# Optimization experiments

Hardware: AMD Instinct MI355X
Metric: run time of the kernel (lower is better)

Reference implementation:

```python
import jax, jax.numpy as jnp
import numpy as np

B, D, N = 32768, 128, 8
TEMP = 0.25          # episodic_memory_temperature
DECAY = 0.99         # episodic_strength_decay
AGE_INC = 0.02       # episodic_age_increment


def _l2norm(x, eps=1e-6):
    n = jnp.sqrt(jnp.sum(x * x, axis=-1, keepdims=True))
    return x / jnp.maximum(n, eps)


def setup_inputs() -> dict:
    key = jax.random.key(0)
    ks = jax.random.split(key, 16)
    s = 0.05
    inp = {
        'signal': jax.random.normal(ks[0], (B, D), jnp.float32),
        'previous': jax.random.normal(ks[1], (B, D), jnp.float32),
        'hidden': jax.random.normal(ks[2], (B, D), jnp.float32),
        'episodic_keys': jax.random.normal(ks[3], (B, N, D), jnp.float32),
        'episodic_values': jax.random.normal(ks[4], (B, N, D), jnp.float32),
        'episodic_strength': jax.random.uniform(ks[5], (B, N), jnp.float32),
        'episodic_age': jax.random.uniform(ks[6], (B, N), jnp.float32),
        # Linear weights stored as [in, out] (torch stores [out, in]); small random
        # instead of the zero init so gradients flow for kernel testing.
        'w_read_query': jax.random.normal(ks[7], (2 * D, D), jnp.float32) * s,
        'w_read_mix': jax.random.normal(ks[8], (2 * D, 1), jnp.float32) * s,
        'b_read_mix': jnp.full((1,), -0.2, jnp.float32),
        'w_key': jax.random.normal(ks[9], (2 * D, D), jnp.float32) * s,
        'b_key': jnp.zeros((D,), jnp.float32),
        'w_value': jax.random.normal(ks[10], (2 * D, D), jnp.float32) * s,
        'b_value': jnp.zeros((D,), jnp.float32),
        'w_write': jax.random.normal(ks[11], (2 * D, 1), jnp.float32) * s,
        'b_write': jnp.full((1,), -0.6, jnp.float32),
        'w_persist': jax.random.normal(ks[12], (2 * D, 1), jnp.float32) * s,
        'b_persist': jnp.zeros((1,), jnp.float32),
        'w_merge': jax.random.normal(ks[13], (2 * D, 1), jnp.float32) * s,
        'b_merge': jnp.zeros((1,), jnp.float32),
    }
    return inp


def reference(signal, previous, hidden, episodic_keys, episodic_values,
              episodic_strength, episodic_age,
              w_read_query, w_read_mix, b_read_mix, w_key, b_key, w_value,
              b_value, w_write, b_write, w_persist, b_persist, w_merge, b_merge):
    dtype = signal.dtype
    n_slots = episodic_keys.shape[1]

    # ---------------- read ----------------
    sp = jnp.concatenate([signal, previous], axis=-1)             # [B, 2D]
    query = _l2norm(sp @ w_read_query)                            # [B, D]
    norm_keys = _l2norm(episodic_keys)                            # [B, N, D]
    content_scores = jnp.einsum('bd,bnd->bn', query, norm_keys)   # [B, N]
    content_w = jax.nn.softmax(content_scores / TEMP, axis=-1)
    content_read = jnp.einsum('bn,bnd->bd', content_w, episodic_values)
    persistent_scores = 2.4 * episodic_strength + 0.6 * (1.0 - episodic_age)
    persistent_w = jax.nn.softmax(persistent_scores / TEMP, axis=-1)
    persistent_read = jnp.einsum('bn,bnd->bd', persistent_w, episodic_values)
    read_mix = jax.nn.sigmoid(sp @ w_read_mix + b_read_mix)       # [B, 1]
    memory_read = read_mix * content_read + (1.0 - read_mix) * persistent_read

    # ---------------- write ----------------
    joined = jnp.concatenate([signal, hidden], axis=-1)           # [B, 2D]
    candidate_key = jnp.tanh(joined @ w_key + b_key)              # [B, D]
    candidate_value = jnp.tanh(joined @ w_value + b_value)        # [B, D]
    write_strength = jax.nn.sigmoid(joined @ w_write + b_write)   # [B, 1]
    persistence = jax.nn.sigmoid(joined @ w_persist + b_persist)  # [B, 1]
    similarity = jnp.einsum('bd,bnd->bn', _l2norm(candidate_key), norm_keys)

    top_k = min(3, n_slots)
    top_sim, top_idx = jax.lax.top_k(similarity, top_k)           # [B, 3]
    max_sim = top_sim[:, 0]
    merge_index = top_idx[:, 0]
    second_sim = top_sim[:, 1]
    novelty = jnp.clip(1.0 - max_sim, 0.0, 1.0)[:, None]          # [B, 1]

    replace_scores = (1.2 * episodic_age + 1.0 * (1.0 - episodic_strength)
                      + 0.5 * (1.0 - similarity))
    replace_index = jnp.argmax(replace_scores, axis=-1)
    merge_pref = jax.nn.sigmoid(joined @ w_merge + b_merge + 2.6 * max_sim[:, None])

    full_m = (max_sim > 0.78) & (merge_pref[:, 0] >= 0.55)
    multi_m = full_m & (second_sim > 0.68)
    partial_m = (~multi_m) & (max_sim > 0.64) & (second_sim > 0.52)

    rows = jnp.arange(signal.shape[0])[:, None]
    target_w = jax.nn.one_hot(replace_index, n_slots, dtype=dtype)
    partial_w = jax.nn.softmax(top_sim[:, :2] / TEMP, axis=-1)
    partial_target = jnp.zeros_like(target_w).at[rows, top_idx[:, :2]].add(partial_w)
    multi_w = jax.nn.softmax(top_sim / TEMP, axis=-1)
    multi_target = jnp.zeros_like(target_w).at[rows, top_idx].add(multi_w)
    full_target = jax.nn.one_hot(merge_index, n_slots, dtype=dtype)

    target_w = jnp.where(full_m[:, None], full_target, target_w)
    target_w = jnp.where(partial_m[:, None], partial_target, target_w)
    target_w = jnp.where(multi_m[:, None], multi_target, target_w)

    scale = jnp.where(multi_m[:, None], 0.16 + 0.52 * write_strength,
                      jnp.where(partial_m[:, None], 0.18 + 0.62 * write_strength,
                                0.20 + 0.80 * write_strength))
    overwrite = target_w * scale * (0.55 + 0.45 * novelty)        # [B, N]
    ow3 = overwrite[..., None]                                    # [B, N, 1]

    merge_like = full_m | partial_m | multi_m
    key_mix = jnp.where(merge_like[:, None], 0.28 + 0.24 * persistence,
                        0.78 + 0.16 * persistence)[:, :, None]    # [B, 1, 1]
    value_mix = jnp.where(merge_like[:, None], 0.42 + 0.28 * persistence,
                          0.82 + 0.12 * persistence)[:, :, None]

    updated_keys = episodic_keys + ow3 * key_mix * (candidate_key[:, None, :] - episodic_keys)
    updated_values = episodic_values + ow3 * value_mix * (candidate_value[:, None, :] - episodic_values)

    boost = overwrite * (0.45 + 0.35 * persistence + 0.45 * novelty + 0.25 * write_strength)
    updated_strength = jnp.clip(episodic_strength * DECAY + boost, 0.0, 1.0)
    updated_age = jnp.clip((episodic_age + AGE_INC) * (1.0 - overwrite), 0.0, 1.0)

    return memory_read, updated_keys, updated_values, updated_strength, updated_age
```

## Files before the change

kernel.cpp:

```cpp
#include <hip/hip_runtime.h>
#include <cstddef>

#define BD 128
#define NS 8
#define ROWS 4
#define BLOCK 256

typedef float __attribute__((ext_vector_type(4))) f32x4;
typedef float __attribute__((ext_vector_type(2))) f32x2;

__device__ __forceinline__ float sigm(float x) { return 1.0f / (1.0f + __expf(-x)); }

__device__ __forceinline__ void nt_store2(float2 v, float2* p) {
    f32x2 t; t.x = v.x; t.y = v.y;
    __builtin_nontemporal_store(t, (f32x2*)p);
}

__global__ __launch_bounds__(BLOCK, 3)
void sbcore_kernel(
    const float* __restrict__ g_signal, const float* __restrict__ g_prev,
    const float* __restrict__ g_hidden, const float* __restrict__ g_keys,
    const float* __restrict__ g_vals, const float* __restrict__ g_str,
    const float* __restrict__ g_age,
    const float* __restrict__ w_rq, const float* __restrict__ w_mix,
    const float* __restrict__ b_mix, const float* __restrict__ w_key,
    const float* __restrict__ b_key, const float* __restrict__ w_val,
    const float* __restrict__ b_val, const float* __restrict__ w_wr,
    const float* __restrict__ b_wr, const float* __restrict__ w_pe,
    const float* __restrict__ b_pe, const float* __restrict__ w_mg,
    const float* __restrict__ b_mg,
    float* __restrict__ o_read, float* __restrict__ o_keys,
    float* __restrict__ o_vals, float* __restrict__ o_str,
    float* __restrict__ o_age)
{
    __shared__ __align__(16) float sig_s[ROWS][BD];
    __shared__ __align__(16) float prv_s[ROWS][BD];
    __shared__ __align__(16) float hid_s[ROWS][BD];
    __shared__ __align__(16) f32x4 part_s[4][3][ROWS][32];
    __shared__ float str_s[ROWS*NS], age_s[ROWS*NS];
    __shared__ __align__(16) float head_s[ROWS][4];

    const int tid = threadIdx.x;
    const int row0 = blockIdx.x * ROWS;

    if (tid < ROWS*32) {
        int r = tid >> 5, d4 = tid & 31;
        size_t gb = (size_t)(row0 + r) * 32 + d4;
        *(float4*)&sig_s[r][d4*4] = ((const float4*)g_signal)[gb];
        *(float4*)&prv_s[r][d4*4] = ((const float4*)g_prev)[gb];
        *(float4*)&hid_s[r][d4*4] = ((const float4*)g_hidden)[gb];
    }
    if (tid < ROWS*NS) {
        str_s[tid] = g_str[(size_t)row0*NS + tid];
        age_s[tid] = g_age[(size_t)row0*NS + tid];
    }
    __syncthreads();

    {
        const int dotid = tid >> 4;
        const int hr = dotid >> 2;
        const int hh = dotid & 3;
        const int hj = tid & 15;
        const float* ws = (hh==0) ? w_mix : (hh==1) ? w_wr : (hh==2) ? w_pe : w_mg;
        const float* xb = (hj < 8) ? &sig_s[hr][0]
                        : (((hh==0) ? &prv_s[hr][0] : &hid_s[hr][0]) - BD);
        float p = 0.f;
#pragma unroll
        for (int q = 0; q < 4; ++q) {
            const int k = hj*16 + q*4;
            const float4 w4 = *(const float4*)&ws[k];
            const float4 x4 = *(const float4*)&xb[k];
            p = fmaf(x4.w, w4.w, fmaf(x4.z, w4.z, fmaf(x4.y, w4.y, fmaf(x4.x, w4.x, p))));
        }
        p += __shfl_xor(p, 1); p += __shfl_xor(p, 2);
        p += __shfl_xor(p, 4); p += __shfl_xor(p, 8);
        if (hj == 0) head_s[hr][hh] = p;
    }

    const int wave = tid >> 6;
    const int lane = tid & 63;
    const int hi   = lane >> 5;
    const int dg   = lane & 31;

    {
        const int kbase = hi ? (BD + wave*32) : (wave*32);
        const f32x4* wq4 = (const f32x4*)w_rq;
        const f32x4* wk4 = (const f32x4*)w_key;
        const f32x4* wv4 = (const f32x4*)w_val;
        const int wi0 = kbase*32 + dg;
        const float* x1b = hi ? &prv_s[0][0] : &sig_s[0][0];
        const float* x2b = hi ? &hid_s[0][0] : &sig_s[0][0];
        const int xo = wave*32;

        f32x4 aq[ROWS], ak[ROWS], av[ROWS];
#pragma unroll
        for (int r = 0; r < ROWS; ++r) { aq[r] = 0.f; ak[r] = 0.f; av[r] = 0.f; }

#pragma unroll 2
        for (int j = 0; j < 8; ++j) {
            const int kj = j*4;
            f32x4 w0 = wq4[wi0 + (kj+0)*32], w1 = wq4[wi0 + (kj+1)*32],
                  w2 = wq4[wi0 + (kj+2)*32], w3 = wq4[wi0 + (kj+3)*32];
#pragma unroll
            for (int r = 0; r < ROWS; ++r) {
                const f32x4 x1 = *(const f32x4*)&x1b[r*BD + xo + kj];
                aq[r] += x1.x*w0; aq[r] += x1.y*w1; aq[r] += x1.z*w2; aq[r] += x1.w*w3;
            }
            f32x4 k0 = wk4[wi0 + (kj+0)*32], k1 = wk4[wi0 + (kj+1)*32],
                  k2 = wk4[wi0 + (kj+2)*32], k3 = wk4[wi0 + (kj+3)*32];
            f32x4 v0 = wv4[wi0 + (kj+0)*32], v1 = wv4[wi0 + (kj+1)*32],
                  v2 = wv4[wi0 + (kj+2)*32], v3 = wv4[wi0 + (kj+3)*32];
#pragma unroll
            for (int r = 0; r < ROWS; ++r) {
                const f32x4 x2 = *(const f32x4*)&x2b[r*BD + xo + kj];
                ak[r] += x2.x*k0; ak[r] += x2.y*k1; ak[r] += x2.z*k2; ak[r] += x2.w*k3;
                av[r] += x2.x*v0; av[r] += x2.y*v1; av[r] += x2.z*v2; av[r] += x2.w*v3;
            }
        }

#pragma unroll
        for (int r = 0; r < ROWS; ++r) {
            f32x4 t;
            t.x = __shfl_xor(aq[r].x, 32); t.y = __shfl_xor(aq[r].y, 32);
            t.z = __shfl_xor(aq[r].z, 32); t.w = __shfl_xor(aq[r].w, 32);
            aq[r] += t;
            t.x = __shfl_xor(ak[r].x, 32); t.y = __shfl_xor(ak[r].y, 32);
            t.z = __shfl_xor(ak[r].z, 32); t.w = __shfl_xor(ak[r].w, 32);
            ak[r] += t;
            t.x = __shfl_xor(av[r].x, 32); t.y = __shfl_xor(av[r].y, 32);
            t.z = __shfl_xor(av[r].z, 32); t.w = __shfl_xor(av[r].w, 32);
            av[r] += t;
        }
        if (!hi) {
#pragma unroll
            for (int r = 0; r < ROWS; ++r) {
                part_s[wave][0][r][dg] = aq[r];
                part_s[wave][1][r][dg] = ak[r];
                part_s[wave][2][r][dg] = av[r];
            }
        }
    }
    __syncthreads();

    const int r = wave;
    float ckinv_reg;
    {
        const int dgf = lane >> 1;
        const int co  = (lane & 1) * 2;
        float2 sq = make_float2(0.f, 0.f), sk = make_float2(0.f, 0.f),
               sv = make_float2(0.f, 0.f);
#pragma unroll
        for (int pw = 0; pw < 4; ++pw) {
            const float* pq = (const float*)&part_s[pw][0][r][dgf];
            const float* pk = (const float*)&part_s[pw][1][r][dgf];
            const float* pv = (const float*)&part_s[pw][2][r][dgf];
            const float2 tq = *(const float2*)&pq[co];
            const float2 tk = *(const float2*)&pk[co];
            const float2 tv = *(const float2*)&pv[co];
            sq.x += tq.x; sq.y += tq.y;
            sk.x += tk.x; sk.y += tk.y;
            sv.x += tv.x; sv.y += tv.y;
        }
        const float2 bk2 = *(const float2*)&b_key[2*lane];
        const float2 bv2 = *(const float2*)&b_val[2*lane];
        const float ckx = tanhf(sk.x + bk2.x), cky = tanhf(sk.y + bk2.y);
        const float cvx = tanhf(sv.x + bv2.x), cvy = tanhf(sv.y + bv2.y);
        float q2 = sq.x*sq.x + sq.y*sq.y;
        float c2 = ckx*ckx + cky*cky;
#pragma unroll
        for (int off = 32; off > 0; off >>= 1) {
            q2 += __shfl_xor(q2, off);
            c2 += __shfl_xor(c2, off);
        }
        const float qinv = 1.0f / fmaxf(sqrtf(q2), 1e-6f);
        ckinv_reg = 1.0f / fmaxf(sqrtf(c2), 1e-6f);
        *(float2*)&sig_s[r][2*lane] = make_float2(sq.x*qinv, sq.y*qinv);
        *(float2*)&prv_s[r][2*lane] = make_float2(ckx, cky);
        *(float2*)&hid_s[r][2*lane] = make_float2(cvx, cvy);
    }
    __syncthreads();

    const float bmix = b_mix[0], bwr = b_wr[0], bpe = b_pe[0], bmg = b_mg[0];
    const int sj = lane & 7;
    {
        const size_t row = (size_t)row0 + r;
        const size_t kvb = row * (size_t)(NS*BD);

        const float4* kp4  = (const float4*)(g_keys + kvb);
        const float4* qrow = (const float4*)&sig_s[r][0];
        const float4* crow = (const float4*)&prv_s[r][0];
        float pk = 0.f, pq = 0.f, pc = 0.f;
#pragma unroll
        for (int q = 0; q < 4; ++q) {
            const float4 k4 = kp4[4*lane + q];
            const float4 q4 = qrow[sj*4 + q];
            const float4 c4 = crow[sj*4 + q];
            pk = fmaf(k4.w,k4.w, fmaf(k4.z,k4.z, fmaf(k4.y,k4.y, fmaf(k4.x,k4.x, pk))));
            pq = fmaf(q4.w,k4.w, fmaf(q4.z,k4.z, fmaf(q4.y,k4.y, fmaf(q4.x,k4.x, pq))));
            pc = fmaf(c4.w,k4.w, fmaf(c4.z,k4.z, fmaf(c4.y,k4.y, fmaf(c4.x,k4.x, pc))));
        }
        const float2* vp = (const float2*)(g_vals + kvb);
        float2 vf[NS];
#pragma unroll
        for (int n = 0; n < NS; ++n) vf[n] = vp[n*64 + lane];
        const float2 cki = *(const float2*)&prv_s[r][2*lane];
        const float2 cvi = *(const float2*)&hid_s[r][2*lane];

        pk += __shfl_xor(pk, 1); pk += __shfl_xor(pk, 2); pk += __shfl_xor(pk, 4);
        pq += __shfl_xor(pq, 1); pq += __shfl_xor(pq, 2); pq += __shfl_xor(pq, 4);
        pc += __shfl_xor(pc, 1); pc += __shfl_xor(pc, 2); pc += __shfl_xor(pc, 4);
        const float ki   = 1.0f / fmaxf(sqrtf(pk), 1e-6f);
        const float csn  = pq * ki;
        const float simn = pc * ki * ckinv_reg;
        float cs[NS], sim[NS];
#pragma unroll
        for (int m = 0; m < NS; ++m) {
            cs[m]  = __shfl(csn,  m*8);
            sim[m] = __shfl(simn, m*8);
        }

        const float4 hd = *(const float4*)&head_s[r][0];
        const float mix   = sigm(hd.x + bmix);
        const float wsv   = sigm(hd.y + bwr);
        const float pev   = sigm(hd.z + bpe);
        const float mglin = hd.w + bmg;

        float mC = cs[0];
#pragma unroll
        for (int n = 1; n < NS; ++n) mC = fmaxf(mC, cs[n]);
        float eC[NS], sC = 0.f;
#pragma unroll
        for (int n = 0; n < NS; ++n) { eC[n] = __expf((cs[n]-mC)*4.0f); sC += eC[n]; }
        const float4 st0 = *(const float4*)&str_s[r*NS];
        const float4 st1 = *(const float4*)&str_s[r*NS+4];
        const float4 ag0 = *(const float4*)&age_s[r*NS];
        const float4 ag1 = *(const float4*)&age_s[r*NS+4];
        const float stv[NS] = {st0.x,st0.y,st0.z,st0.w,st1.x,st1.y,st1.z,st1.w};
        const float agv[NS] = {ag0.x,ag0.y,ag0.z,ag0.w,ag1.x,ag1.y,ag1.z,ag1.w};
        float psc[NS]; float mP = -1e30f;
#pragma unroll
        for (int n = 0; n < NS; ++n) {
            psc[n] = fmaf(2.4f, stv[n], 0.6f*(1.0f - agv[n]));
            mP = fmaxf(mP, psc[n]);
        }
        float eP[NS], sP = 0.f;
#pragma unroll
        for (int n = 0; n < NS; ++n) { eP[n] = __expf((psc[n]-mP)*4.0f); sP += eP[n]; }
        const float icS = 1.0f/sC, ipS = 1.0f/sP;

        float2 cr = make_float2(0.f, 0.f), prd = make_float2(0.f, 0.f);
#pragma unroll
        for (int n = 0; n < NS; ++n) {
            float wc = eC[n]*icS, wp = eP[n]*ipS;
            cr.x  = fmaf(wc, vf[n].x, cr.x);  cr.y  = fmaf(wc, vf[n].y, cr.y);
            prd.x = fmaf(wp, vf[n].x, prd.x); prd.y = fmaf(wp, vf[n].y, prd.y);
        }
        float2 mr;
        mr.x = mix*cr.x + (1.0f-mix)*prd.x;
        mr.y = mix*cr.y + (1.0f-mix)*prd.y;
        nt_store2(mr, &((float2*)(o_read + row*BD))[lane]);

        float tv0 = -1e30f; int ti0 = 0;
#pragma unroll
        for (int n = 0; n < NS; ++n) if (sim[n] > tv0) { tv0 = sim[n]; ti0 = n; }
        float tv1 = -1e30f; int ti1 = 0;
#pragma unroll
        for (int n = 0; n < NS; ++n) {
            float v = (n == ti0) ? -1e30f : sim[n];
            if (v > tv1) { tv1 = v; ti1 = n; }
        }
        float tv2 = -1e30f; int ti2 = 0;
#pragma unroll
        for (int n = 0; n < NS; ++n) {
            float v = (n == ti0 || n == ti1) ? -1e30f : sim[n];
            if (v > tv2) { tv2 = v; ti2 = n; }
        }

        float rm = -1e30f; int ri = 0;
#pragma unroll
        for (int n = 0; n < NS; ++n) {
            float rsv = fmaf(1.2f, agv[n], (1.0f - stv[n])) + 0.5f*(1.0f - sim[n]);
            if (rsv > rm) { rm = rsv; ri = n; }
        }

        const float mpref = sigm(mglin + 2.6f*tv0);
        const bool full  = (tv0 > 0.78f) && (mpref >= 0.55f);
        const bool multi = full && (tv1 > 0.68f);
        const bool part  = (!multi) && (tv0 > 0.64f) && (tv1 > 0.52f);
        const float nov  = fminf(fmaxf(1.0f - tv0, 0.0f), 1.0f);

        float a0, a1, a2, aR;
        if (multi) {
            float e1 = __expf((tv1 - tv0)*4.0f), e2 = __expf((tv2 - tv0)*4.0f);
            float inv = 1.0f/(1.0f + e1 + e2);
            a0 = inv; a1 = e1*inv; a2 = e2*inv; aR = 0.f;
        } else if (part) {
            float e1 = __expf((tv1 - tv0)*4.0f);
            float inv = 1.0f/(1.0f + e1);
            a0 = inv; a1 = e1*inv; a2 = 0.f; aR = 0.f;
        } else if (full) {
            a0 = 1.f; a1 = 0.f; a2 = 0.f; aR = 0.f;
        } else {
            a0 = 0.f; a1 = 0.f; a2 = 0.f; aR = 1.f;
        }

        const float scl = multi ? fmaf(0.52f, wsv, 0.16f)
                        : part  ? fmaf(0.62f, wsv, 0.18f)
                                : fmaf(0.80f, wsv, 0.20f);
        const bool  mlike = full || part || multi;
        const float km  = mlike ? fmaf(0.24f, pev, 0.28f) : fmaf(0.16f, pev, 0.78f);
        const float vm  = mlike ? fmaf(0.28f, pev, 0.42f) : fmaf(0.12f, pev, 0.82f);
        const float owc = scl * fmaf(0.45f, nov, 0.55f);
        const float bco = 0.45f + 0.35f*pev + 0.45f*nov + 0.25f*wsv;

        const float2* kp2 = (const float2*)(g_keys + kvb);
        float2* okp = (float2*)(o_keys + kvb);
        float2* ovp = (float2*)(o_vals + kvb);
#pragma unroll
        for (int n = 0; n < NS; ++n) {
            const float2 kf2 = kp2[n*64 + lane];
            float tn = ((n==ti0) ? a0 : (n==ti1) ? a1 : (n==ti2) ? a2 : 0.f)
                     + ((n==ri) ? aR : 0.f);
            float ow = tn*owc;
            float a = ow*km, b2 = ow*vm;
            float2 uk, uv;
            uk.x = fmaf(a,  cki.x - kf2.x, kf2.x);
            uk.y = fmaf(a,  cki.y - kf2.y, kf2.y);
            uv.x = fmaf(b2, cvi.x - vf[n].x, vf[n].x);
            uv.y = fmaf(b2, cvi.y - vf[n].y, vf[n].y);
            nt_store2(uk, &okp[n*64 + lane]);
            nt_store2(uv, &ovp[n*64 + lane]);
        }
        if (lane < NS) {
            float tn = ((lane==ti0) ? a0 : (lane==ti1) ? a1 : (lane==ti2) ? a2 : 0.f)
                     + ((lane==ri) ? aR : 0.f);
            float ow = tn*owc;
            float us = fminf(fmaxf(fmaf(str_s[r*NS+lane], 0.99f, ow*bco), 0.f), 1.f);
            float ua = fminf(fmaxf((age_s[r*NS+lane] + 0.02f)*(1.0f - ow), 0.f), 1.f);
            o_str[row*NS + lane] = us;
            o_age[row*NS + lane] = ua;
        }
    }
}

extern "C" void kernel_launch(void* const* d_in, const int* in_sizes, int n_in,
                              void* d_out, int out_size, void* d_ws, size_t ws_size,
                              hipStream_t stream) {
    const float* g_signal = (const float*)d_in[0];
    const float* g_prev   = (const float*)d_in[1];
    const float* g_hidden = (const float*)d_in[2];
    const float* g_keys   = (const float*)d_in[3];
    const float* g_vals   = (const float*)d_in[4];
    const float* g_str    = (const float*)d_in[5];
    const float* g_age    = (const float*)d_in[6];
    const float* w_rq     = (const float*)d_in[7];
    const float* w_mix    = (const float*)d_in[8];
    const float* b_mix    = (const float*)d_in[9];
    const float* w_key    = (const float*)d_in[10];
    const float* b_key    = (const float*)d_in[11];
    const float* w_val    = (const float*)d_in[12];
    const float* b_val    = (const float*)d_in[13];
    const float* w_wr     = (const float*)d_in[14];
    const float* b_wr     = (const float*)d_in[15];
    const float* w_pe     = (const float*)d_in[16];
    const float* b_pe     = (const float*)d_in[17];
    const float* w_mg     = (const float*)d_in[18];
    const float* b_mg     = (const float*)d_in[19];

    const size_t B = (size_t)in_sizes[0] / BD;
    float* out   = (float*)d_out;
    float* o_read = out;
    float* o_keys = o_read + B*BD;
    float* o_vals = o_keys + B*NS*BD;
    float* o_str  = o_vals + B*NS*BD;
    float* o_age  = o_str  + B*NS;

    const int blocks = (int)(B / ROWS);
    sbcore_kernel<<<dim3(blocks), dim3(BLOCK), 0, stream>>>(
        g_signal, g_prev, g_hidden, g_keys, g_vals, g_str, g_age,
        w_rq, w_mix, b_mix, w_key, b_key, w_val, b_val,
        w_wr, b_wr, w_pe, b_pe, w_mg, b_mg,
        o_read, o_keys, o_vals, o_str, o_age);
}
```

Measured before the change: 613.3 us.

## Split fused kernel into matvec and slot-update kernels via workspace

Splits the single fused kernel into two: one computes the query/key/value projections, head logits and inverse norms into a workspace, and the other streams the episodic keys and values to do slot scoring, read and update. The fused kernel is kept as a fallback when no workspace is provided. The aim is to let each phase use its own resource profile (occupancy, memory streaming) instead of mixing compute-heavy matvec with bandwidth-bound slot traffic. It adds a workspace round trip of about 389 floats per row plus an extra launch.

```diff
diff --git a/kernel.cpp b/kernel.cpp
--- a/kernel.cpp
+++ b/kernel.cpp
@@ -17,7 +17,340 @@
 }
 
 __global__ __launch_bounds__(BLOCK, 3)
-void sbcore_kernel(
+void sbcore_matvec(
+    const float* __restrict__ g_signal, const float* __restrict__ g_prev,
+    const float* __restrict__ g_hidden,
+    const float* __restrict__ w_rq, const float* __restrict__ w_mix,
+    const float* __restrict__ w_key, const float* __restrict__ b_key,
+    const float* __restrict__ w_val, const float* __restrict__ b_val,
+    const float* __restrict__ w_wr, const float* __restrict__ w_pe,
+    const float* __restrict__ w_mg,
+    float* __restrict__ ws_qcv, float* __restrict__ ws_heads,
+    float* __restrict__ ws_ckinv)
+{
+    __shared__ __align__(16) float sig_s[ROWS][BD];
+    __shared__ __align__(16) float prv_s[ROWS][BD];
+    __shared__ __align__(16) float hid_s[ROWS][BD];
+    __shared__ __align__(16) f32x4 part_s[4][3][ROWS][32];
+
+    const int tid = threadIdx.x;
+    const int row0 = blockIdx.x * ROWS;
+    const int wave = tid >> 6;
+    const int lane = tid & 63;
+
+    if (tid < ROWS*32) {
+        int r = tid >> 5, d4 = tid & 31;
+        size_t gb = (size_t)(row0 + r) * 32 + d4;
+        *(float4*)&sig_s[r][d4*4] = ((const float4*)g_signal)[gb];
+        *(float4*)&prv_s[r][d4*4] = ((const float4*)g_prev)[gb];
+        *(float4*)&hid_s[r][d4*4] = ((const float4*)g_hidden)[gb];
+    }
+    __syncthreads();
+
+    {
+        const int dotid = tid >> 4;
+        const int hr = dotid >> 2;
+        const int hh = dotid & 3;
+        const int hj = tid & 15;
+        const float* ws = (hh==0) ? w_mix : (hh==1) ? w_wr : (hh==2) ? w_pe : w_mg;
+        const float* xb = (hj < 8) ? &sig_s[hr][0]
+                        : (((hh==0) ? &prv_s[hr][0] : &hid_s[hr][0]) - BD);
+        float p = 0.f;
+#pragma unroll
+        for (int q = 0; q < 4; ++q) {
+            const int k = hj*16 + q*4;
+            const float4 w4 = *(const float4*)&ws[k];
+            const float4 x4 = *(const float4*)&xb[k];
+            p = fmaf(x4.w, w4.w, fmaf(x4.z, w4.z, fmaf(x4.y, w4.y, fmaf(x4.x, w4.x, p))));
+        }
+        p += __shfl_xor(p, 1); p += __shfl_xor(p, 2);
+        p += __shfl_xor(p, 4); p += __shfl_xor(p, 8);
+        if (hj == 0) ws_heads[(size_t)(row0 + hr)*4 + hh] = p;
+    }
+
+    const int hi = lane >> 5;
+    const int dg = lane & 31;
+
+    {
+        const int kbase = hi ? (BD + wave*32) : (wave*32);
+        const f32x4* wq4 = (const f32x4*)w_rq;
+        const f32x4* wk4 = (const f32x4*)w_key;
+        const f32x4* wv4 = (const f32x4*)w_val;
+        const int wi0 = kbase*32 + dg;
+        const float* x1b = hi ? &prv_s[0][0] : &sig_s[0][0];
+        const float* x2b = hi ? &hid_s[0][0] : &sig_s[0][0];
+        const int xo = wave*32;
+
+        f32x4 aq[ROWS], ak[ROWS], av[ROWS];
+#pragma unroll
+        for (int r = 0; r < ROWS; ++r) { aq[r] = 0.f; ak[r] = 0.f; av[r] = 0.f; }
+
+#pragma unroll 2
+        for (int j = 0; j < 8; ++j) {
+            const int kj = j*4;
+            f32x4 w0 = wq4[wi0 + (kj+0)*32], w1 = wq4[wi0 + (kj+1)*32],
+                  w2 = wq4[wi0 + (kj+2)*32], w3 = wq4[wi0 + (kj+3)*32];
+#pragma unroll
+            for (int r = 0; r < ROWS; ++r) {
+                const f32x4 x1 = *(const f32x4*)&x1b[r*BD + xo + kj];
+                aq[r] += x1.x*w0; aq[r] += x1.y*w1; aq[r] += x1.z*w2; aq[r] += x1.w*w3;
+            }
+            f32x4 k0 = wk4[wi0 + (kj+0)*32], k1 = wk4[wi0 + (kj+1)*32],
+                  k2 = wk4[wi0 + (kj+2)*32], k3 = wk4[wi0 + (kj+3)*32];
+            f32x4 v0 = wv4[wi0 + (kj+0)*32], v1 = wv4[wi0 + (kj+1)*32],
+                  v2 = wv4[wi0 + (kj+2)*32], v3 = wv4[wi0 + (kj+3)*32];
+#pragma unroll
+            for (int r = 0; r < ROWS; ++r) {
+                const f32x4 x2 = *(const f32x4*)&x2b[r*BD + xo + kj];
+                ak[r] += x2.x*k0; ak[r] += x2.y*k1; ak[r] += x2.z*k2; ak[r] += x2.w*k3;
+                av[r] += x2.x*v0; av[r] += x2.y*v1; av[r] += x2.z*v2; av[r] += x2.w*v3;
+            }
+        }
+
+#pragma unroll
+        for (int r = 0; r < ROWS; ++r) {
+            f32x4 t;
+            t.x = __shfl_xor(aq[r].x, 32); t.y = __shfl_xor(aq[r].y, 32);
+            t.z = __shfl_xor(aq[r].z, 32); t.w = __shfl_xor(aq[r].w, 32);
+            aq[r] += t;
+            t.x = __shfl_xor(ak[r].x, 32); t.y = __shfl_xor(ak[r].y, 32);
+            t.z = __shfl_xor(ak[r].z, 32); t.w = __shfl_xor(ak[r].w, 32);
+            ak[r] += t;
+            t.x = __shfl_xor(av[r].x, 32); t.y = __shfl_xor(av[r].y, 32);
+            t.z = __shfl_xor(av[r].z, 32); t.w = __shfl_xor(av[r].w, 32);
+            av[r] += t;
+        }
+        if (!hi) {
+#pragma unroll
+            for (int r = 0; r < ROWS; ++r) {
+                part_s[wave][0][r][dg] = aq[r];
+                part_s[wave][1][r][dg] = ak[r];
+                part_s[wave][2][r][dg] = av[r];
+            }
+        }
+    }
+    __syncthreads();
+
+    const int r = wave;
+    {
+        const int dgf = lane >> 1;
+        const int co  = (lane & 1) * 2;
+        float2 sq = make_float2(0.f, 0.f), sk = make_float2(0.f, 0.f),
+               sv = make_float2(0.f, 0.f);
+#pragma unroll
+        for (int pw = 0; pw < 4; ++pw) {
+            const float* pq = (const float*)&part_s[pw][0][r][dgf];
+            const float* pk = (const float*)&part_s[pw][1][r][dgf];
+            const float* pv = (const float*)&part_s[pw][2][r][dgf];
+            const float2 tq = *(const float2*)&pq[co];
+            const float2 tk = *(const float2*)&pk[co];
+            const float2 tv = *(const float2*)&pv[co];
+            sq.x += tq.x; sq.y += tq.y;
+            sk.x += tk.x; sk.y += tk.y;
+            sv.x += tv.x; sv.y += tv.y;
+        }
+        const float2 bk2 = *(const float2*)&b_key[2*lane];
+        const float2 bv2 = *(const float2*)&b_val[2*lane];
+        const float ckx = tanhf(sk.x + bk2.x), cky = tanhf(sk.y + bk2.y);
+        const float cvx = tanhf(sv.x + bv2.x), cvy = tanhf(sv.y + bv2.y);
+        float q2 = sq.x*sq.x + sq.y*sq.y;
+        float c2 = ckx*ckx + cky*cky;
+#pragma unroll
+        for (int off = 32; off > 0; off >>= 1) {
+            q2 += __shfl_xor(q2, off);
+            c2 += __shfl_xor(c2, off);
+        }
+        const float qinv = 1.0f / fmaxf(sqrtf(q2), 1e-6f);
+        const size_t rowb = ((size_t)row0 + r) * 384;
+        *(float2*)&ws_qcv[rowb + 2*lane]       = make_float2(sq.x*qinv, sq.y*qinv);
+        *(float2*)&ws_qcv[rowb + 128 + 2*lane] = make_float2(ckx, cky);
+        *(float2*)&ws_qcv[rowb + 256 + 2*lane] = make_float2(cvx, cvy);
+        if (lane == 0) ws_ckinv[(size_t)row0 + r] = 1.0f / fmaxf(sqrtf(c2), 1e-6f);
+    }
+}
+
+__global__ __launch_bounds__(BLOCK, 2)
+void sbcore_slots(
+    const float* __restrict__ ws_qcv, const float* __restrict__ ws_heads,
+    const float* __restrict__ ws_ckinv,
+    const float* __restrict__ g_keys, const float* __restrict__ g_vals,
+    const float* __restrict__ g_str, const float* __restrict__ g_age,
+    const float* __restrict__ b_mix, const float* __restrict__ b_wr,
+    const float* __restrict__ b_pe, const float* __restrict__ b_mg,
+    float* __restrict__ o_read, float* __restrict__ o_keys,
+    float* __restrict__ o_vals, float* __restrict__ o_str,
+    float* __restrict__ o_age)
+{
+    const int tid  = threadIdx.x;
+    const int wave = tid >> 6;
+    const int lane = tid & 63;
+    const int sj   = lane & 7;
+    const size_t row = (size_t)blockIdx.x * ROWS + wave;
+    const size_t kvb = row * (size_t)(NS*BD);
+
+    const float* wsrow = ws_qcv + row*384;
+    const float4* qrow = (const float4*)wsrow;
+    const float4* crow = (const float4*)(wsrow + 128);
+    const float4* kp4  = (const float4*)(g_keys + kvb);
+    const float2* vp2  = (const float2*)(g_vals + kvb);
+
+    float pk = 0.f, pq = 0.f, pc = 0.f;
+#pragma unroll
+    for (int q = 0; q < 4; ++q) {
+        const float4 k4 = kp4[4*lane + q];
+        const float4 q4 = qrow[sj*4 + q];
+        const float4 c4 = crow[sj*4 + q];
+        pk = fmaf(k4.w,k4.w, fmaf(k4.z,k4.z, fmaf(k4.y,k4.y, fmaf(k4.x,k4.x, pk))));
+        pq = fmaf(q4.w,k4.w, fmaf(q4.z,k4.z, fmaf(q4.y,k4.y, fmaf(q4.x,k4.x, pq))));
+        pc = fmaf(c4.w,k4.w, fmaf(c4.z,k4.z, fmaf(c4.y,k4.y, fmaf(c4.x,k4.x, pc))));
+    }
+    float2 vf[NS];
+#pragma unroll
+    for (int n = 0; n < NS; ++n) vf[n] = vp2[n*64 + lane];
+    const float2 cki = ((const float2*)(wsrow + 128))[lane];
+    const float2 cvi = ((const float2*)(wsrow + 256))[lane];
+
+    pk += __shfl_xor(pk, 1); pk += __shfl_xor(pk, 2); pk += __shfl_xor(pk, 4);
+    pq += __shfl_xor(pq, 1); pq += __shfl_xor(pq, 2); pq += __shfl_xor(pq, 4);
+    pc += __shfl_xor(pc, 1); pc += __shfl_xor(pc, 2); pc += __shfl_xor(pc, 4);
+    const float ki    = 1.0f / fmaxf(sqrtf(pk), 1e-6f);
+    const float ckinv = ws_ckinv[row];
+    const float csn   = pq * ki;
+    const float simn  = pc * ki * ckinv;
+    float cs[NS], sim[NS];
+#pragma unroll
+    for (int m = 0; m < NS; ++m) {
+        cs[m]  = __shfl(csn,  m*8);
+        sim[m] = __shfl(simn, m*8);
+    }
+
+    const float4 hd = *(const float4*)&ws_heads[row*4];
+    const float mix   = sigm(hd.x + b_mix[0]);
+    const float wsv   = sigm(hd.y + b_wr[0]);
+    const float pev   = sigm(hd.z + b_pe[0]);
+    const float mglin = hd.w + b_mg[0];
+
+    float mC = cs[0];
+#pragma unroll
+    for (int n = 1; n < NS; ++n) mC = fmaxf(mC, cs[n]);
+    float eC[NS], sC = 0.f;
+#pragma unroll
+    for (int n = 0; n < NS; ++n) { eC[n] = __expf((cs[n]-mC)*4.0f); sC += eC[n]; }
+    const float4 st0 = *(const float4*)&g_str[row*NS];
+    const float4 st1 = *(const float4*)&g_str[row*NS+4];
+    const float4 ag0 = *(const float4*)&g_age[row*NS];
+    const float4 ag1 = *(const float4*)&g_age[row*NS+4];
+    const float stv[NS] = {st0.x,st0.y,st0.z,st0.w,st1.x,st1.y,st1.z,st1.w};
+    const float agv[NS] = {ag0.x,ag0.y,ag0.z,ag0.w,ag1.x,ag1.y,ag1.z,ag1.w};
+    float psc[NS]; float mP = -1e30f;
+#pragma unroll
+    for (int n = 0; n < NS; ++n) {
+        psc[n] = fmaf(2.4f, stv[n], 0.6f*(1.0f - agv[n]));
+        mP = fmaxf(mP, psc[n]);
+    }
+    float eP[NS], sP = 0.f;
+#pragma unroll
+    for (int n = 0; n < NS; ++n) { eP[n] = __expf((psc[n]-mP)*4.0f); sP += eP[n]; }
+    const float icS = 1.0f/sC, ipS = 1.0f/sP;
+
+    float2 cr = make_float2(0.f, 0.f), prd = make_float2(0.f, 0.f);
+#pragma unroll
+    for (int n = 0; n < NS; ++n) {
+        float wc = eC[n]*icS, wp = eP[n]*ipS;
+        cr.x  = fmaf(wc, vf[n].x, cr.x);  cr.y  = fmaf(wc, vf[n].y, cr.y);
+        prd.x = fmaf(wp, vf[n].x, prd.x); prd.y = fmaf(wp, vf[n].y, prd.y);
+    }
+    float2 mr;
+    mr.x = mix*cr.x + (1.0f-mix)*prd.x;
+    mr.y = mix*cr.y + (1.0f-mix)*prd.y;
+    nt_store2(mr, &((float2*)(o_read + row*BD))[lane]);
+
+    float tv0 = -1e30f; int ti0 = 0;
+#pragma unroll
+    for (int n = 0; n < NS; ++n) if (sim[n] > tv0) { tv0 = sim[n]; ti0 = n; }
+    float tv1 = -1e30f; int ti1 = 0;
+#pragma unroll
+    for (int n = 0; n < NS; ++n) {
+        float v = (n == ti0) ? -1e30f : sim[n];
+        if (v > tv1) { tv1 = v; ti1 = n; }
+    }
+    float tv2 = -1e30f; int ti2 = 0;
+#pragma unroll
+    for (int n = 0; n < NS; ++n) {
+        float v = (n == ti0 || n == ti1) ? -1e30f : sim[n];
+        if (v > tv2) { tv2 = v; ti2 = n; }
+    }
+
+    float rm = -1e30f; int ri = 0;
+#pragma unroll
+    for (int n = 0; n < NS; ++n) {
+        float rsv = fmaf(1.2f, agv[n], (1.0f - stv[n])) + 0.5f*(1.0f - sim[n]);
+        if (rsv > rm) { rm = rsv; ri = n; }
+    }
+
+    const float mpref = sigm(mglin + 2.6f*tv0);
+    const bool full  = (tv0 > 0.78f) && (mpref >= 0.55f);
+    const bool multi = full && (tv1 > 0.68f);
+    const bool part  = (!multi) && (tv0 > 0.64f) && (tv1 > 0.52f);
+    const float nov  = fminf(fmaxf(1.0f - tv0, 0.0f), 1.0f);
+
+    float a0, a1, a2, aR;
+    if (multi) {
+        float e1 = __expf((tv1 - tv0)*4.0f), e2 = __expf((tv2 - tv0)*4.0f);
+        float inv = 1.0f/(1.0f + e1 + e2);
+        a0 = inv; a1 = e1*inv; a2 = e2*inv; aR = 0.f;
+    } else if (part) {
+        float e1 = __expf((tv1 - tv0)*4.0f);
+        float inv = 1.0f/(1.0f + e1);
+        a0 = inv; a1 = e1*inv; a2 = 0.f; aR = 0.f;
+    } else if (full) {
+        a0 = 1.f; a1 = 0.f; a2 = 0.f; aR = 0.f;
+    } else {
+        a0 = 0.f; a1 = 0.f; a2 = 0.f; aR = 1.f;
+    }
+
+    const float scl = multi ? fmaf(0.52f, wsv, 0.16f)
+                    : part  ? fmaf(0.62f, wsv, 0.18f)
+                            : fmaf(0.80f, wsv, 0.20f);
+    const bool  mlike = full || part || multi;
+    const float km  = mlike ? fmaf(0.24f, pev, 0.28f) : fmaf(0.16f, pev, 0.78f);
+    const float vm  = mlike ? fmaf(0.28f, pev, 0.42f) : fmaf(0.12f, pev, 0.82f);
+    const float owc = scl * fmaf(0.45f, nov, 0.55f);
+    const float bco = 0.45f + 0.35f*pev + 0.45f*nov + 0.25f*wsv;
+
+    const float2* kp2 = (const float2*)(g_keys + kvb);
+    float2* okp = (float2*)(o_keys + kvb);
+    float2* ovp = (float2*)(o_vals + kvb);
+#pragma unroll
+    for (int n = 0; n < NS; ++n) {
+        const float2 kf2 = kp2[n*64 + lane];
+        float tn = ((n==ti0) ? a0 : (n==ti1) ? a1 : (n==ti2) ? a2 : 0.f)
+                 + ((n==ri) ? aR : 0.f);
+        float ow = tn*owc;
+        float a = ow*km, b2 = ow*vm;
+        float2 uk, uv;
+        uk.x = fmaf(a,  cki.x - kf2.x, kf2.x);
+        uk.y = fmaf(a,  cki.y - kf2.y, kf2.y);
+        uv.x = fmaf(b2, cvi.x - vf[n].x, vf[n].x);
+        uv.y = fmaf(b2, cvi.y - vf[n].y, vf[n].y);
+        nt_store2(uk, &okp[n*64 + lane]);
+        nt_store2(uv, &ovp[n*64 + lane]);
+    }
+    if (lane < NS) {
+        float tn = ((lane==ti0) ? a0 : (lane==ti1) ? a1 : (lane==ti2) ? a2 : 0.f)
+                 + ((lane==ri) ? aR : 0.f);
+        float ow = tn*owc;
+        float s0 = g_str[row*NS + lane];
+        float g0 = g_age[row*NS + lane];
+        float us = fminf(fmaxf(fmaf(s0, 0.99f, ow*bco), 0.f), 1.f);
+        float ua = fminf(fmaxf((g0 + 0.02f)*(1.0f - ow), 0.f), 1.f);
+        o_str[row*NS + lane] = us;
+        o_age[row*NS + lane] = ua;
+    }
+}
+
+__global__ __launch_bounds__(BLOCK, 3)
+void sbcore_fused(
     const float* __restrict__ g_signal, const float* __restrict__ g_prev,
     const float* __restrict__ g_hidden, const float* __restrict__ g_keys,
     const float* __restrict__ g_vals, const float* __restrict__ g_str,
@@ -79,8 +412,8 @@
 
     const int wave = tid >> 6;
     const int lane = tid & 63;
-    const int hi   = lane >> 5;
-    const int dg   = lane & 31;
+    const int hi = lane >> 5;
+    const int dg = lane & 31;
 
     {
         const int kbase = hi ? (BD + wave*32) : (wave*32);
@@ -367,18 +700,35 @@
     const float* w_mg     = (const float*)d_in[18];
     const float* b_mg     = (const float*)d_in[19];
 
-    const size_t B = (size_t)in_sizes[0] / BD;
+    const size_t Bn = (size_t)in_sizes[0] / BD;
     float* out   = (float*)d_out;
     float* o_read = out;
-    float* o_keys = o_read + B*BD;
-    float* o_vals = o_keys + B*NS*BD;
-    float* o_str  = o_vals + B*NS*BD;
-    float* o_age  = o_str  + B*NS;
-
-    const int blocks = (int)(B / ROWS);
-    sbcore_kernel<<<dim3(blocks), dim3(BLOCK), 0, stream>>>(
-        g_signal, g_prev, g_hidden, g_keys, g_vals, g_str, g_age,
-        w_rq, w_mix, b_mix, w_key, b_key, w_val, b_val,
-        w_wr, b_wr, w_pe, b_pe, w_mg, b_mg,
-        o_read, o_keys, o_vals, o_str, o_age);
+    float* o_keys = o_read + Bn*BD;
+    float* o_vals = o_keys + Bn*NS*BD;
+    float* o_str  = o_vals + Bn*NS*BD;
+    float* o_age  = o_str  + Bn*NS;
+
+    const int blocks = (int)(Bn / ROWS);
+    const size_t needed = Bn * (size_t)(384 + 4 + 1) * sizeof(float);
+
+    if (d_ws != nullptr && ws_size >= needed) {
+        float* ws_qcv   = (float*)d_ws;
+        float* ws_heads = ws_qcv + Bn*384;
+        float* ws_ckinv = ws_heads + Bn*4;
+        sbcore_matvec<<<dim3(blocks), dim3(BLOCK), 0, stream>>>(
+            g_signal, g_prev, g_hidden,
+            w_rq, w_mix, w_key, b_key, w_val, b_val, w_wr, w_pe, w_mg,
+            ws_qcv, ws_heads, ws_ckinv);
+        sbcore_slots<<<dim3(blocks), dim3(BLOCK), 0, stream>>>(
+            ws_qcv, ws_heads, ws_ckinv,
+            g_keys, g_vals, g_str, g_age,
+            b_mix, b_wr, b_pe, b_mg,
+            o_read, o_keys, o_vals, o_str, o_age);
+    } else {
+        sbcore_fused<<<dim3(blocks), dim3(BLOCK), 0, stream>>>(
+            g_signal, g_prev, g_hidden, g_keys, g_vals, g_str, g_age,
+            w_rq, w_mix, b_mix, w_key, b_key, w_val, b_val,
+            w_wr, b_wr, w_pe, b_pe, w_mg, b_mg,
+            o_read, o_keys, o_vals, o_str, o_age);
+    }
 }
```

Result: slower. 653.4 us (+6.5%).
